# Kernel optimization log

Hardware: AMD Instinct MI355X
Metric: run time of the kernel (lower is better)

Reference implementation:

```python
import jax, jax.numpy as jnp
import numpy as np

NUM_SLOTS = 24
EPS = 1e-5

def setup_inputs() -> dict:
    key = jax.random.key(0)
    k1, k2 = jax.random.split(key)
    x = jax.random.normal(k1, (4, 32, 200, 2048), dtype=jnp.float32)
    time = jax.random.randint(k2, (4, 2048), 0, NUM_SLOTS, dtype=jnp.int64)
    return {"x": x, "time": time}

def reference(x, time):
    # x: [b, c, n, t]; time: [b, t] int slot ids in [0, NUM_SLOTS)
    b, c, n, t = x.shape
    time = time[..., -t:]
    idx = time.reshape(b * t)

    # [b*t, n, c] layout matching x.permute(2,0,3,1).reshape(n, b*t, c) contraction
    xf = jnp.transpose(x, (0, 3, 2, 1)).reshape(b * t, n * c)

    # True segment-sum replaces the one-hot matmul; column L1-normalize == divide by slot count
    counts = jax.ops.segment_sum(jnp.ones((b * t,), x.dtype), idx, num_segments=NUM_SLOTS)
    denom = jnp.maximum(counts, 1e-12)[:, None]  # F.normalize eps-clamped norm

    sum_x = jax.ops.segment_sum(xf, idx, num_segments=NUM_SLOTS)            # [S, n*c]
    sum_x2 = jax.ops.segment_sum(xf * xf, idx, num_segments=NUM_SLOTS)      # [S, n*c]

    mean_slot = (sum_x / denom).reshape(NUM_SLOTS, n, c).mean(axis=1)       # [S, c]
    m2_slot = (sum_x2 / denom).reshape(NUM_SLOTS, n, c).mean(axis=1)        # [S, c]
    var_slot = m2_slot - mean_slot ** 2                                     # [S, c]

    # Embedding gather back per (b, t), broadcast over n
    sm = jnp.transpose(mean_slot[time], (0, 2, 1))[:, :, None, :]           # [b, c, 1, t]
    sv = jnp.transpose(var_slot[time], (0, 2, 1))[:, :, None, :]            # [b, c, 1, t]

    return (x - sm) / jnp.sqrt(sv + EPS)
```

## Files before the change

### kernel.cpp

```cpp
#include <hip/hip_runtime.h>
#include <math.h>

#define Bb 4
#define Cc 32
#define Nn 200
#define Tt 2048
#define Ss 24
#define EPSf 1e-5f
#define GRID 512
#define RKEEP 40

typedef float f4 __attribute__((ext_vector_type(4)));
typedef int i4 __attribute__((ext_vector_type(4)));
typedef unsigned u4 __attribute__((ext_vector_type(4)));

__device__ __forceinline__ unsigned rne_bf16(float f) {
    unsigned u = __float_as_uint(f);
    return (u + 0x7FFFu + ((u >> 16) & 1u)) >> 16;
}
__device__ __forceinline__ unsigned pack2(float a, float b) {
    return rne_bf16(a) | (rne_bf16(b) << 16);
}
__device__ __forceinline__ float lo16(unsigned u) { return __uint_as_float(u << 16); }
__device__ __forceinline__ float hi16(unsigned u) { return __uint_as_float(u & 0xFFFF0000u); }


__global__ void k_zero(int* __restrict__ counter) { *counter = 0; }

#define ROWS40(M) M(0) M(1) M(2) M(3) M(4) M(5) M(6) M(7) M(8) M(9) \
                  M(10) M(11) M(12) M(13) M(14) M(15) M(16) M(17) M(18) M(19) \
                  M(20) M(21) M(22) M(23) M(24) M(25) M(26) M(27) M(28) M(29) \
                  M(30) M(31) M(32) M(33) M(34) M(35) M(36) M(37) M(38) M(39)

#define DROW(i) u4 xb##i;

#define LROW(i) { \
    f4 v0 = *(const f4*)(bp + (size_t)(i) * Tt); \
    f4 v1 = *(const f4*)(bp + (size_t)(i) * Tt + 1024); \
    xb##i[0] = pack2(v0[0], v0[1]); \
    xb##i[1] = pack2(v0[2], v0[3]); \
    xb##i[2] = pack2(v1[0], v1[1]); \
    xb##i[3] = pack2(v1[2], v1[3]); \
    s0 += v0[0]; q0 += v0[0]*v0[0]; s1 += v0[1]; q1 += v0[1]*v0[1]; \
    s2 += v0[2]; q2 += v0[2]*v0[2]; s3 += v0[3]; q3 += v0[3]*v0[3]; \
    s4 += v1[0]; q4 += v1[0]*v1[0]; s5 += v1[1]; q5 += v1[1]*v1[1]; \
    s6 += v1[2]; q6 += v1[2]*v1[2]; s7 += v1[3]; q7 += v1[3]*v1[3]; }

#define SROW(i) { \
    f4 o0, o1; \
    o0[0] = fmaf(lo16(xb##i[0]), rr0, -mr0); \
    o0[1] = fmaf(hi16(xb##i[0]), rr1, -mr1); \
    o0[2] = fmaf(lo16(xb##i[1]), rr2, -mr2); \
    o0[3] = fmaf(hi16(xb##i[1]), rr3, -mr3); \
    o1[0] = fmaf(lo16(xb##i[2]), rr4, -mr4); \
    o1[1] = fmaf(hi16(xb##i[2]), rr5, -mr5); \
    o1[2] = fmaf(lo16(xb##i[3]), rr6, -mr6); \
    o1[3] = fmaf(hi16(xb##i[3]), rr7, -mr7); \
    __builtin_nontemporal_store(o0, (f4*)(op + (size_t)(i) * Tt)); \
    __builtin_nontemporal_store(o1, (f4*)(op + (size_t)(i) * Tt + 1024)); }

__attribute__((amdgpu_waves_per_eu(2, 2)))
__global__ __launch_bounds__(256) void k_fused(const float* __restrict__ x,
                                               const int* __restrict__ timei,
                                               float2* __restrict__ part,
                                               int* __restrict__ cntp,
                                               int* __restrict__ counter,
                                               float* __restrict__ out) {
    __shared__ float lsum[Ss], lsq[Ss];
    __shared__ int   lcnt[Ss];
    __shared__ float s_r[Ss], s_mr[Ss];

    const int tid = threadIdx.x;
    const int bx  = blockIdx.x;
    const int b   = bx >> 7;
    const int c   = (bx >> 2) & 31;
    const int q   = bx & 3;
    const bool do_hist = (c == 0 && q == 0);

    if (tid < Ss) { lsum[tid] = 0.f; lsq[tid] = 0.f; lcnt[tid] = 0; }
    __syncthreads();

    const int t0 = tid * 4;
    const i4 sl0 = *(const i4*)(timei + b * Tt + t0);
    const i4 sl1 = *(const i4*)(timei + b * Tt + t0 + 1024);

    const size_t plane = ((size_t)(b * Cc + c) * Nn + (size_t)q * 50) * Tt;
    const float* bp = x + plane + t0;

    ROWS40(DROW)
    float s0=0,s1=0,s2=0,s3=0,s4=0,s5=0,s6=0,s7=0;
    float q0=0,q1=0,q2=0,q3=0,q4=0,q5=0,q6=0,q7=0;

    ROWS40(LROW)
    for (int r = RKEEP; r < 50; ++r) {
        f4 v0 = *(const f4*)(bp + (size_t)r * Tt);
        f4 v1 = *(const f4*)(bp + (size_t)r * Tt + 1024);
        s0 += v0[0]; q0 += v0[0]*v0[0]; s1 += v0[1]; q1 += v0[1]*v0[1];
        s2 += v0[2]; q2 += v0[2]*v0[2]; s3 += v0[3]; q3 += v0[3]*v0[3];
        s4 += v1[0]; q4 += v1[0]*v1[0]; s5 += v1[1]; q5 += v1[1]*v1[1];
        s6 += v1[2]; q6 += v1[2]*v1[2]; s7 += v1[3]; q7 += v1[3]*v1[3];
    }

    atomicAdd(&lsum[sl0[0]], s0); atomicAdd(&lsq[sl0[0]], q0);
    atomicAdd(&lsum[sl0[1]], s1); atomicAdd(&lsq[sl0[1]], q1);
    atomicAdd(&lsum[sl0[2]], s2); atomicAdd(&lsq[sl0[2]], q2);
    atomicAdd(&lsum[sl0[3]], s3); atomicAdd(&lsq[sl0[3]], q3);
    atomicAdd(&lsum[sl1[0]], s4); atomicAdd(&lsq[sl1[0]], q4);
    atomicAdd(&lsum[sl1[1]], s5); atomicAdd(&lsq[sl1[1]], q5);
    atomicAdd(&lsum[sl1[2]], s6); atomicAdd(&lsq[sl1[2]], q6);
    atomicAdd(&lsum[sl1[3]], s7); atomicAdd(&lsq[sl1[3]], q7);
    if (do_hist) {
        atomicAdd(&lcnt[sl0[0]], 1); atomicAdd(&lcnt[sl0[1]], 1);
        atomicAdd(&lcnt[sl0[2]], 1); atomicAdd(&lcnt[sl0[3]], 1);
        atomicAdd(&lcnt[sl1[0]], 1); atomicAdd(&lcnt[sl1[1]], 1);
        atomicAdd(&lcnt[sl1[2]], 1); atomicAdd(&lcnt[sl1[3]], 1);
    }
    __syncthreads();

    if (tid < Ss) {
        part[(c * Ss + tid) * 16 + (b * 4 + q)] = make_float2(lsum[tid], lsq[tid]);
        if (do_hist) cntp[b * Ss + tid] = lcnt[tid];
    }
    __syncthreads();

    if (tid == 0) {
        __threadfence();
        __hip_atomic_fetch_add(counter, 1, __ATOMIC_ACQ_REL, __HIP_MEMORY_SCOPE_AGENT);
        while (__hip_atomic_load(counter, __ATOMIC_ACQUIRE, __HIP_MEMORY_SCOPE_AGENT) < GRID)
            __builtin_amdgcn_s_sleep(2);
        __threadfence();
    }
    __syncthreads();

    if (tid < Ss) { lsum[tid] = 0.f; lsq[tid] = 0.f; }
    __syncthreads();
    if (tid < 192) {
        const int s = tid >> 3, j = tid & 7;
        float2 p0 = part[(c * Ss + s) * 16 + 2 * j];
        float2 p1 = part[(c * Ss + s) * 16 + 2 * j + 1];
        atomicAdd(&lsum[s], p0.x + p1.x);
        atomicAdd(&lsq[s],  p0.y + p1.y);
    }
    __syncthreads();
    if (tid < Ss) {
        int cnt = cntp[tid] + cntp[Ss + tid] + cntp[2 * Ss + tid] + cntp[3 * Ss + tid];
        float denom = fmaxf((float)cnt, 1e-12f) * (float)Nn;
        float m  = lsum[tid] / denom;
        float m2 = lsq[tid]  / denom;
        float rr = 1.0f / sqrtf(m2 - m * m + EPSf);
        s_r[tid]  = rr;
        s_mr[tid] = m * rr;
    }
    __syncthreads();

    const float rr0 = s_r[sl0[0]], mr0 = s_mr[sl0[0]];
    const float rr1 = s_r[sl0[1]], mr1 = s_mr[sl0[1]];
    const float rr2 = s_r[sl0[2]], mr2 = s_mr[sl0[2]];
    const float rr3 = s_r[sl0[3]], mr3 = s_mr[sl0[3]];
    const float rr4 = s_r[sl1[0]], mr4 = s_mr[sl1[0]];
    const float rr5 = s_r[sl1[1]], mr5 = s_mr[sl1[1]];
    const float rr6 = s_r[sl1[2]], mr6 = s_mr[sl1[2]];
    const float rr7 = s_r[sl1[3]], mr7 = s_mr[sl1[3]];

    float* op = out + plane + t0;
    ROWS40(SROW)
    for (int r = RKEEP; r < 50; ++r) {
        f4 v0 = *(const f4*)(bp + (size_t)r * Tt);
        f4 v1 = *(const f4*)(bp + (size_t)r * Tt + 1024);
        f4 o0, o1;
        o0[0] = fmaf(v0[0], rr0, -mr0);
        o0[1] = fmaf(v0[1], rr1, -mr1);
        o0[2] = fmaf(v0[2], rr2, -mr2);
        o0[3] = fmaf(v0[3], rr3, -mr3);
        o1[0] = fmaf(v1[0], rr4, -mr4);
        o1[1] = fmaf(v1[1], rr5, -mr5);
        o1[2] = fmaf(v1[2], rr6, -mr6);
        o1[3] = fmaf(v1[3], rr7, -mr7);
        __builtin_nontemporal_store(o0, (f4*)(op + (size_t)r * Tt));
        __builtin_nontemporal_store(o1, (f4*)(op + (size_t)r * Tt + 1024));
    }
}

__global__ __launch_bounds__(256) void k_stats(const float* __restrict__ x,
                                               const int* __restrict__ timei,
                                               float2* __restrict__ part,
                                               int* __restrict__ cntpart) {
    __shared__ float lsum[Ss], lsq[Ss];
    __shared__ int   lcnt[Ss];
    const int tid = threadIdx.x;
    const int bx  = blockIdx.x;
    const int tt = bx & 1;
    const int nc = (bx >> 1) & 7;
    const int bc = bx >> 4;
    const int b  = bc >> 5;
    const int c  = bc & 31;
    const bool do_hist = (c == 0 && nc == 0);

    if (tid < Ss) { lsum[tid] = 0.f; lsq[tid] = 0.f; lcnt[tid] = 0; }
    __syncthreads();

    const int t0 = tt * 1024 + tid * 4;
    const i4 sl = *(const i4*)(timei + b * Tt + t0);

    const size_t plane = ((size_t)(b * Cc + c) * Nn + (size_t)nc * 25) * Tt;
    const float* bp = x + plane + t0;

    float s0 = 0.f, s1 = 0.f, s2 = 0.f, s3 = 0.f;
    float q0 = 0.f, q1 = 0.f, q2 = 0.f, q3 = 0.f;
#pragma unroll 5
    for (int r = 0; r < 25; ++r) {
        f4 v = *(const f4*)(bp + (size_t)r * Tt);
        s0 += v[0]; q0 += v[0] * v[0];
        s1 += v[1]; q1 += v[1] * v[1];
        s2 += v[2]; q2 += v[2] * v[2];
        s3 += v[3]; q3 += v[3] * v[3];
    }

    atomicAdd(&lsum[sl[0]], s0); atomicAdd(&lsq[sl[0]], q0);
    atomicAdd(&lsum[sl[1]], s1); atomicAdd(&lsq[sl[1]], q1);
    atomicAdd(&lsum[sl[2]], s2); atomicAdd(&lsq[sl[2]], q2);
    atomicAdd(&lsum[sl[3]], s3); atomicAdd(&lsq[sl[3]], q3);
    if (do_hist) {
        atomicAdd(&lcnt[sl[0]], 1); atomicAdd(&lcnt[sl[1]], 1);
        atomicAdd(&lcnt[sl[2]], 1); atomicAdd(&lcnt[sl[3]], 1);
    }
    __syncthreads();

    const int chunk = (b * 2 + tt) * 8 + nc;
    if (tid < Ss) {
        part[(c * Ss + tid) * 64 + chunk] = make_float2(lsum[tid], lsq[tid]);
        if (do_hist) cntpart[(b * 2 + tt) * Ss + tid] = lcnt[tid];
    }
}

__global__ __launch_bounds__(256) void k_norm(const float* __restrict__ x,
                                              const int* __restrict__ timei,
                                              const float2* __restrict__ part,
                                              const int* __restrict__ cntpart,
                                              float* __restrict__ out) {
    __shared__ float lsum[Ss], lsq[Ss];
    __shared__ float s_mr[Ss], s_r[Ss];
    const int tid = threadIdx.x;
    const int bx  = blockIdx.x;
    const int b  = bx >> 7;
    const int c  = (bx >> 2) & 31;
    const int nc = bx & 3;

    if (tid < Ss) { lsum[tid] = 0.f; lsq[tid] = 0.f; }
    __syncthreads();
    if (tid < 192) {
        const int s = tid >> 3, j = tid & 7;
        const float2* pp = &part[(c * Ss + s) * 64 + j * 8];
        float ps = 0.f, pq = 0.f;
#pragma unroll
        for (int k = 0; k < 8; ++k) { ps += pp[k].x; pq += pp[k].y; }
        atomicAdd(&lsum[s], ps);
        atomicAdd(&lsq[s],  pq);
    }
    __syncthreads();
    if (tid < Ss) {
        int cnt = 0;
#pragma unroll
        for (int h = 0; h < 8; ++h) cnt += cntpart[h * Ss + tid];
        float denom = fmaxf((float)cnt, 1e-12f) * (float)Nn;
        float m  = lsum[tid] / denom;
        float m2 = lsq[tid]  / denom;
        float rr = 1.0f / sqrtf(m2 - m * m + EPSf);
        s_r[tid]  = rr;
        s_mr[tid] = m * rr;
    }
    __syncthreads();

    const int t0 = tid * 4;
    const i4 sl0 = *(const i4*)(timei + b * Tt + t0);
    const i4 sl1 = *(const i4*)(timei + b * Tt + t0 + 1024);
    const float rr0 = s_r[sl0[0]], mr0 = s_mr[sl0[0]];
    const float rr1 = s_r[sl0[1]], mr1 = s_mr[sl0[1]];
    const float rr2 = s_r[sl0[2]], mr2 = s_mr[sl0[2]];
    const float rr3 = s_r[sl0[3]], mr3 = s_mr[sl0[3]];
    const float rr4 = s_r[sl1[0]], mr4 = s_mr[sl1[0]];
    const float rr5 = s_r[sl1[1]], mr5 = s_mr[sl1[1]];
    const float rr6 = s_r[sl1[2]], mr6 = s_mr[sl1[2]];
    const float rr7 = s_r[sl1[3]], mr7 = s_mr[sl1[3]];

    const size_t plane = ((size_t)(b * Cc + c) * Nn + (size_t)nc * 50) * Tt;
    const float* xp = x + plane + t0;
    float* op = out + plane + t0;

#pragma unroll 5
    for (int r = 0; r < 50; ++r) {
        f4 v0 = *(const f4*)(xp + (size_t)r * Tt);
        f4 v1 = *(const f4*)(xp + (size_t)r * Tt + 1024);
        f4 o0, o1;
        o0[0] = fmaf(v0[0], rr0, -mr0);
        o0[1] = fmaf(v0[1], rr1, -mr1);
        o0[2] = fmaf(v0[2], rr2, -mr2);
        o0[3] = fmaf(v0[3], rr3, -mr3);
        o1[0] = fmaf(v1[0], rr4, -mr4);
        o1[1] = fmaf(v1[1], rr5, -mr5);
        o1[2] = fmaf(v1[2], rr6, -mr6);
        o1[3] = fmaf(v1[3], rr7, -mr7);
        __builtin_nontemporal_store(o0, (f4*)(op + (size_t)r * Tt));
        __builtin_nontemporal_store(o1, (f4*)(op + (size_t)r * Tt + 1024));
    }
}

extern "C" void kernel_launch(void* const* d_in, const int* in_sizes, int n_in,
                              void* d_out, int out_size, void* d_ws, size_t ws_size,
                              hipStream_t stream) {
    const float* x   = (const float*)d_in[0];
    const int* timei = (const int*)d_in[1];
    float* out = (float*)d_out;

    hipFuncAttributes fa;
    bool fused_ok = (hipFuncGetAttributes(&fa, (const void*)k_fused) == hipSuccess)
                    && fa.localSizeBytes == 0;

    if (fused_ok) {
        float2* part = (float2*)d_ws;
        int* cntp    = (int*)((char*)d_ws + (size_t)Cc * Ss * 16 * sizeof(float2));
        int* counter = (int*)((char*)d_ws + (size_t)Cc * Ss * 16 * sizeof(float2)
                              + 128 * sizeof(int));
        k_zero<<<1, 1, 0, stream>>>(counter);
        k_fused<<<GRID, 256, 0, stream>>>(x, timei, part, cntp, counter, out);
    } else {
        float2* part = (float2*)d_ws;
        int* cnt = (int*)((char*)d_ws + (size_t)Cc * Ss * 64 * sizeof(float2));
        k_stats<<<2048, 256, 0, stream>>>(x, timei, part, cnt);
        k_norm<<<512, 256, 0, stream>>>(x, timei, part, cnt, out);
    }
}
```

Baseline: 104.0 us.

## Split fused kernel rows across two thread groups and stage overflow rows in LDS

The fused single-pass kernel now launches 512 threads per block instead of 256. Each half of the block covers 25 of the block's 50 rows, and each thread handles 8 contiguous time steps rather than two strided groups of 4. Sixteen rows are kept in registers as packed bf16, and the remaining nine go into a shared-memory buffer. This removes the second global read of x for the rows that previously did not fit in registers. The cost is about 72KB of LDS per block and a new host-side occupancy check that falls back to the two-kernel path unless two blocks fit per CU.

```diff
diff --git a/kernel.cpp b/kernel.cpp
--- a/kernel.cpp
+++ b/kernel.cpp
@@ -7,8 +7,7 @@
 #define Tt 2048
 #define Ss 24
 #define EPSf 1e-5f
-#define GRID 512
-#define RKEEP 40
+#define GRID2 512
 
 typedef float f4 __attribute__((ext_vector_type(4)));
 typedef int i4 __attribute__((ext_vector_type(4)));
@@ -27,24 +26,22 @@
 
 __global__ void k_zero(int* __restrict__ counter) { *counter = 0; }
 
-#define ROWS40(M) M(0) M(1) M(2) M(3) M(4) M(5) M(6) M(7) M(8) M(9) \
-                  M(10) M(11) M(12) M(13) M(14) M(15) M(16) M(17) M(18) M(19) \
-                  M(20) M(21) M(22) M(23) M(24) M(25) M(26) M(27) M(28) M(29) \
-                  M(30) M(31) M(32) M(33) M(34) M(35) M(36) M(37) M(38) M(39)
+#define ROWS16(M) M(0) M(1) M(2) M(3) M(4) M(5) M(6) M(7) \
+                  M(8) M(9) M(10) M(11) M(12) M(13) M(14) M(15)
 
 #define DROW(i) u4 xb##i;
 
 #define LROW(i) { \
     f4 v0 = *(const f4*)(bp + (size_t)(i) * Tt); \
-    f4 v1 = *(const f4*)(bp + (size_t)(i) * Tt + 1024); \
+    f4 v1 = *(const f4*)(bp + (size_t)(i) * Tt + 4); \
     xb##i[0] = pack2(v0[0], v0[1]); \
     xb##i[1] = pack2(v0[2], v0[3]); \
     xb##i[2] = pack2(v1[0], v1[1]); \
     xb##i[3] = pack2(v1[2], v1[3]); \
-    s0 += v0[0]; q0 += v0[0]*v0[0]; s1 += v0[1]; q1 += v0[1]*v0[1]; \
-    s2 += v0[2]; q2 += v0[2]*v0[2]; s3 += v0[3]; q3 += v0[3]*v0[3]; \
-    s4 += v1[0]; q4 += v1[0]*v1[0]; s5 += v1[1]; q5 += v1[1]*v1[1]; \
-    s6 += v1[2]; q6 += v1[2]*v1[2]; s7 += v1[3]; q7 += v1[3]*v1[3]; }
+    s0 += v0[0]; a0 += v0[0]*v0[0]; s1 += v0[1]; a1 += v0[1]*v0[1]; \
+    s2 += v0[2]; a2 += v0[2]*v0[2]; s3 += v0[3]; a3 += v0[3]*v0[3]; \
+    s4 += v1[0]; a4 += v1[0]*v1[0]; s5 += v1[1]; a5 += v1[1]*v1[1]; \
+    s6 += v1[2]; a6 += v1[2]*v1[2]; s7 += v1[3]; a7 += v1[3]*v1[3]; }
 
 #define SROW(i) { \
     f4 o0, o1; \
@@ -57,15 +54,15 @@
     o1[2] = fmaf(lo16(xb##i[3]), rr6, -mr6); \
     o1[3] = fmaf(hi16(xb##i[3]), rr7, -mr7); \
     __builtin_nontemporal_store(o0, (f4*)(op + (size_t)(i) * Tt)); \
-    __builtin_nontemporal_store(o1, (f4*)(op + (size_t)(i) * Tt + 1024)); }
-
-__attribute__((amdgpu_waves_per_eu(2, 2)))
-__global__ __launch_bounds__(256) void k_fused(const float* __restrict__ x,
+    __builtin_nontemporal_store(o1, (f4*)(op + (size_t)(i) * Tt + 4)); }
+
+__global__ __launch_bounds__(512) void k_fused(const float* __restrict__ x,
                                                const int* __restrict__ timei,
                                                float2* __restrict__ part,
                                                int* __restrict__ cntp,
                                                int* __restrict__ counter,
                                                float* __restrict__ out) {
+    __shared__ unsigned ldsd[9 * 4 * 512];
     __shared__ float lsum[Ss], lsq[Ss];
     __shared__ int   lcnt[Ss];
     __shared__ float s_r[Ss], s_mr[Ss];
@@ -74,42 +71,47 @@
     const int bx  = blockIdx.x;
     const int b   = bx >> 7;
     const int c   = (bx >> 2) & 31;
-    const int q   = bx & 3;
-    const bool do_hist = (c == 0 && q == 0);
+    const int qc  = bx & 3;
+    const int rg  = tid >> 8;
+    const int t0  = (tid & 255) * 8;
 
     if (tid < Ss) { lsum[tid] = 0.f; lsq[tid] = 0.f; lcnt[tid] = 0; }
     __syncthreads();
 
-    const int t0 = tid * 4;
     const i4 sl0 = *(const i4*)(timei + b * Tt + t0);
-    const i4 sl1 = *(const i4*)(timei + b * Tt + t0 + 1024);
-
-    const size_t plane = ((size_t)(b * Cc + c) * Nn + (size_t)q * 50) * Tt;
-    const float* bp = x + plane + t0;
-
-    ROWS40(DROW)
+    const i4 sl1 = *(const i4*)(timei + b * Tt + t0 + 4);
+
+    const size_t plane = ((size_t)(b * Cc + c) * Nn + (size_t)qc * 50 + (size_t)rg * 25) * Tt + t0;
+    const float* bp = x + plane;
+
+    ROWS16(DROW)
     float s0=0,s1=0,s2=0,s3=0,s4=0,s5=0,s6=0,s7=0;
-    float q0=0,q1=0,q2=0,q3=0,q4=0,q5=0,q6=0,q7=0;
-
-    ROWS40(LROW)
-    for (int r = RKEEP; r < 50; ++r) {
+    float a0=0,a1=0,a2=0,a3=0,a4=0,a5=0,a6=0,a7=0;
+
+    ROWS16(LROW)
+    for (int r = 16; r < 25; ++r) {
         f4 v0 = *(const f4*)(bp + (size_t)r * Tt);
-        f4 v1 = *(const f4*)(bp + (size_t)r * Tt + 1024);
-        s0 += v0[0]; q0 += v0[0]*v0[0]; s1 += v0[1]; q1 += v0[1]*v0[1];
-        s2 += v0[2]; q2 += v0[2]*v0[2]; s3 += v0[3]; q3 += v0[3]*v0[3];
-        s4 += v1[0]; q4 += v1[0]*v1[0]; s5 += v1[1]; q5 += v1[1]*v1[1];
-        s6 += v1[2]; q6 += v1[2]*v1[2]; s7 += v1[3]; q7 += v1[3]*v1[3];
-    }
-
-    atomicAdd(&lsum[sl0[0]], s0); atomicAdd(&lsq[sl0[0]], q0);
-    atomicAdd(&lsum[sl0[1]], s1); atomicAdd(&lsq[sl0[1]], q1);
-    atomicAdd(&lsum[sl0[2]], s2); atomicAdd(&lsq[sl0[2]], q2);
-    atomicAdd(&lsum[sl0[3]], s3); atomicAdd(&lsq[sl0[3]], q3);
-    atomicAdd(&lsum[sl1[0]], s4); atomicAdd(&lsq[sl1[0]], q4);
-    atomicAdd(&lsum[sl1[1]], s5); atomicAdd(&lsq[sl1[1]], q5);
-    atomicAdd(&lsum[sl1[2]], s6); atomicAdd(&lsq[sl1[2]], q6);
-    atomicAdd(&lsum[sl1[3]], s7); atomicAdd(&lsq[sl1[3]], q7);
-    if (do_hist) {
+        f4 v1 = *(const f4*)(bp + (size_t)r * Tt + 4);
+        const int base = (r - 16) * 4 * 512 + tid;
+        ldsd[base]        = pack2(v0[0], v0[1]);
+        ldsd[base + 512]  = pack2(v0[2], v0[3]);
+        ldsd[base + 1024] = pack2(v1[0], v1[1]);
+        ldsd[base + 1536] = pack2(v1[2], v1[3]);
+        s0 += v0[0]; a0 += v0[0]*v0[0]; s1 += v0[1]; a1 += v0[1]*v0[1];
+        s2 += v0[2]; a2 += v0[2]*v0[2]; s3 += v0[3]; a3 += v0[3]*v0[3];
+        s4 += v1[0]; a4 += v1[0]*v1[0]; s5 += v1[1]; a5 += v1[1]*v1[1];
+        s6 += v1[2]; a6 += v1[2]*v1[2]; s7 += v1[3]; a7 += v1[3]*v1[3];
+    }
+
+    atomicAdd(&lsum[sl0[0]], s0); atomicAdd(&lsq[sl0[0]], a0);
+    atomicAdd(&lsum[sl0[1]], s1); atomicAdd(&lsq[sl0[1]], a1);
+    atomicAdd(&lsum[sl0[2]], s2); atomicAdd(&lsq[sl0[2]], a2);
+    atomicAdd(&lsum[sl0[3]], s3); atomicAdd(&lsq[sl0[3]], a3);
+    atomicAdd(&lsum[sl1[0]], s4); atomicAdd(&lsq[sl1[0]], a4);
+    atomicAdd(&lsum[sl1[1]], s5); atomicAdd(&lsq[sl1[1]], a5);
+    atomicAdd(&lsum[sl1[2]], s6); atomicAdd(&lsq[sl1[2]], a6);
+    atomicAdd(&lsum[sl1[3]], s7); atomicAdd(&lsq[sl1[3]], a7);
+    if (c == 0 && qc == 0 && rg == 0) {
         atomicAdd(&lcnt[sl0[0]], 1); atomicAdd(&lcnt[sl0[1]], 1);
         atomicAdd(&lcnt[sl0[2]], 1); atomicAdd(&lcnt[sl0[3]], 1);
         atomicAdd(&lcnt[sl1[0]], 1); atomicAdd(&lcnt[sl1[1]], 1);
@@ -118,15 +120,15 @@
     __syncthreads();
 
     if (tid < Ss) {
-        part[(c * Ss + tid) * 16 + (b * 4 + q)] = make_float2(lsum[tid], lsq[tid]);
-        if (do_hist) cntp[b * Ss + tid] = lcnt[tid];
+        part[(c * Ss + tid) * 16 + (b * 4 + qc)] = make_float2(lsum[tid], lsq[tid]);
+        if (c == 0 && qc == 0) cntp[b * Ss + tid] = lcnt[tid];
     }
     __syncthreads();
 
     if (tid == 0) {
         __threadfence();
         __hip_atomic_fetch_add(counter, 1, __ATOMIC_ACQ_REL, __HIP_MEMORY_SCOPE_AGENT);
-        while (__hip_atomic_load(counter, __ATOMIC_ACQUIRE, __HIP_MEMORY_SCOPE_AGENT) < GRID)
+        while (__hip_atomic_load(counter, __ATOMIC_ACQUIRE, __HIP_MEMORY_SCOPE_AGENT) < GRID2)
             __builtin_amdgcn_s_sleep(2);
         __threadfence();
     }
@@ -162,22 +164,25 @@
     const float rr6 = s_r[sl1[2]], mr6 = s_mr[sl1[2]];
     const float rr7 = s_r[sl1[3]], mr7 = s_mr[sl1[3]];
 
-    float* op = out + plane + t0;
-    ROWS40(SROW)
-    for (int r = RKEEP; r < 50; ++r) {
-        f4 v0 = *(const f4*)(bp + (size_t)r * Tt);
-        f4 v1 = *(const f4*)(bp + (size_t)r * Tt + 1024);
+    float* op = out + plane;
+    ROWS16(SROW)
+    for (int r = 16; r < 25; ++r) {
+        const int base = (r - 16) * 4 * 512 + tid;
+        const unsigned w0 = ldsd[base];
+        const unsigned w1 = ldsd[base + 512];
+        const unsigned w2 = ldsd[base + 1024];
+        const unsigned w3 = ldsd[base + 1536];
         f4 o0, o1;
-        o0[0] = fmaf(v0[0], rr0, -mr0);
-        o0[1] = fmaf(v0[1], rr1, -mr1);
-        o0[2] = fmaf(v0[2], rr2, -mr2);
-        o0[3] = fmaf(v0[3], rr3, -mr3);
-        o1[0] = fmaf(v1[0], rr4, -mr4);
-        o1[1] = fmaf(v1[1], rr5, -mr5);
-        o1[2] = fmaf(v1[2], rr6, -mr6);
-        o1[3] = fmaf(v1[3], rr7, -mr7);
+        o0[0] = fmaf(lo16(w0), rr0, -mr0);
+        o0[1] = fmaf(hi16(w0), rr1, -mr1);
+        o0[2] = fmaf(lo16(w1), rr2, -mr2);
+        o0[3] = fmaf(hi16(w1), rr3, -mr3);
+        o1[0] = fmaf(lo16(w2), rr4, -mr4);
+        o1[1] = fmaf(hi16(w2), rr5, -mr5);
+        o1[2] = fmaf(lo16(w3), rr6, -mr6);
+        o1[3] = fmaf(hi16(w3), rr7, -mr7);
         __builtin_nontemporal_store(o0, (f4*)(op + (size_t)r * Tt));
-        __builtin_nontemporal_store(o1, (f4*)(op + (size_t)r * Tt + 1024));
+        __builtin_nontemporal_store(o1, (f4*)(op + (size_t)r * Tt + 4));
     }
 }
 
@@ -315,14 +320,19 @@
     hipFuncAttributes fa;
     bool fused_ok = (hipFuncGetAttributes(&fa, (const void*)k_fused) == hipSuccess)
                     && fa.localSizeBytes == 0;
+    if (fused_ok) {
+        int occ = 0;
+        fused_ok = (hipOccupancyMaxActiveBlocksPerMultiprocessor(&occ, k_fused, 512, 0)
+                    == hipSuccess) && occ >= 2;
+    }
 
     if (fused_ok) {
         float2* part = (float2*)d_ws;
-        int* cntp    = (int*)((char*)d_ws + (size_t)Cc * Ss * 16 * sizeof(float2));
-        int* counter = (int*)((char*)d_ws + (size_t)Cc * Ss * 16 * sizeof(float2)
+        int* cntp    = (int*)((char*)d_ws + (size_t)Cc * Ss * 64 * sizeof(float2));
+        int* counter = (int*)((char*)d_ws + (size_t)Cc * Ss * 64 * sizeof(float2)
                               + 128 * sizeof(int));
         k_zero<<<1, 1, 0, stream>>>(counter);
-        k_fused<<<GRID, 256, 0, stream>>>(x, timei, part, cntp, counter, out);
+        k_fused<<<GRID2, 512, 0, stream>>>(x, timei, part, cntp, counter, out);
     } else {
         float2* part = (float2*)d_ws;
         int* cnt = (int*)((char*)d_ws + (size_t)Cc * Ss * 64 * sizeof(float2));
```

New measurement: 104.0 us. Within noise of the previous version (-0.0%).
